# Performance work log

Measured on AMD Instinct MI355X. Metric: run time of the kernel, lower is better.

The kernel has to match this reference:

```python
import jax, jax.numpy as jnp
import numpy as np

EPS = 1e-7  # tf.keras.backend.epsilon()
ROUTINGS = 3


def squash(s):
    # s: [B, J, D]
    n2 = jnp.sum(s * s, axis=-1, keepdims=True) + EPS
    return (n2 / (1.0 + n2)) * s / jnp.sqrt(n2)


def setup_inputs() -> dict:
    key = jax.random.key(0)
    k1, k2 = jax.random.split(key)
    B, I, P = 64, 2048, 16   # batch, input_num_capsules, input_dim_capsules
    J, D = 32, 16            # num_capsules, dim_capsules (must equal P per source matmul)
    inputs = jax.random.normal(k1, (B, I, P), dtype=jnp.float32)
    W = jax.random.normal(k2, (I, J, P, D), dtype=jnp.float32) * 0.05  # glorot-ish scale
    return {"inputs": inputs, "W": W}


def reference(inputs, W):
    # tf.matmul(W_tiled, inputs_tiled): u_hat[b,i,j,d] = sum_p W[i,j,d,p] * inputs[b,i,p]
    u_hat = jnp.einsum('bip,ijdp->bijd', inputs, W)  # [B, I, J, D]
    B, I, J, _ = u_hat.shape
    b = jnp.zeros((B, I, J), dtype=u_hat.dtype)
    v = None
    for r in range(ROUTINGS):
        c = jax.nn.softmax(b, axis=2)                  # [B, I, J]
        s = jnp.einsum('bij,bijd->bjd', c, u_hat)      # [B, J, D]
        v = squash(s)
        if r < ROUTINGS - 1:
            b = b + jnp.einsum('bijd,bjd->bij', u_hat, v)
    return v
```

## Files before the change

### kernel.cpp

```cpp
#include <hip/hip_runtime.h>
#include <hip/hip_bf16.h>
#include <stdint.h>


namespace {
constexpr int B_ = 64;
constexpr int I_ = 2048;
constexpr int P_ = 16;
constexpr int J_ = 32;
constexpr int D_ = 16;
constexpr int CI_ = 128;

__device__ __forceinline__ float bflo(uint32_t v) {
  union { uint32_t u; float f; } z; z.u = v << 16; return z.f;
}
__device__ __forceinline__ float bfhi(uint32_t v) {
  union { uint32_t u; float f; } z; z.u = v & 0xffff0000u; return z.f;
}

__global__ __launch_bounds__(256) void k_uhat(const float* __restrict__ x,
                                              const float* __restrict__ W,
                                              __hip_bfloat162* __restrict__ uhat) {
  const int i = blockIdx.x;
  const int t = threadIdx.x;
  __shared__ float xs[B_][P_];
  {
    const int b = t >> 2, c = t & 3;
    const float4 v = *reinterpret_cast<const float4*>(
        x + (size_t)b * (I_ * P_) + (size_t)i * P_ + c * 4);
    *reinterpret_cast<float4*>(&xs[b][c * 4]) = v;
  }
  float w0[P_], w1[P_];
  const float* Wi = W + (size_t)i * (J_ * D_ * P_);
#pragma unroll
  for (int c = 0; c < 4; ++c) {
    *reinterpret_cast<float4*>(&w0[c * 4]) =
        *reinterpret_cast<const float4*>(Wi + (2 * t + 0) * P_ + c * 4);
    *reinterpret_cast<float4*>(&w1[c * 4]) =
        *reinterpret_cast<const float4*>(Wi + (2 * t + 1) * P_ + c * 4);
  }
  __syncthreads();
  __hip_bfloat162* dst = uhat + (size_t)i * (J_ * D_ / 2) + t;
#pragma unroll 4
  for (int b = 0; b < B_; ++b) {
    const float4* xb = reinterpret_cast<const float4*>(&xs[b][0]);
    const float4 x0 = xb[0], x1 = xb[1], x2 = xb[2], x3 = xb[3];
    const float xr[P_] = {x0.x, x0.y, x0.z, x0.w, x1.x, x1.y, x1.z, x1.w,
                          x2.x, x2.y, x2.z, x2.w, x3.x, x3.y, x3.z, x3.w};
    float a0 = 0.f, a1 = 0.f;
#pragma unroll
    for (int p = 0; p < P_; ++p) {
      a0 = fmaf(xr[p], w0[p], a0);
      a1 = fmaf(xr[p], w1[p], a1);
    }
    __hip_bfloat162 pk;
    pk.x = __float2bfloat16(a0);
    pk.y = __float2bfloat16(a1);
    dst[(size_t)b * (I_ * J_ * D_ / 2)] = pk;
  }
}

__global__ __launch_bounds__(256) void k_route(const uint4* __restrict__ uhat,
                                               const float* __restrict__ vsum,
                                               float* __restrict__ s) {
  const int b = blockIdx.y;
  const int i0 = blockIdx.x * CI_;
  const int t = threadIdx.x;
  const int lane = t & 63;
  const int wave = t >> 6;
  const int sub = lane >> 5;
  const int j = lane & 31;

  float vr[D_];
  {
    const float4* vp = reinterpret_cast<const float4*>(vsum + ((size_t)b * J_ + j) * D_);
#pragma unroll
    for (int c = 0; c < 4; ++c) {
      const float4 v = vp[c];
      vr[c * 4 + 0] = v.x; vr[c * 4 + 1] = v.y;
      vr[c * 4 + 2] = v.z; vr[c * 4 + 3] = v.w;
    }
  }
  float acc[D_];
#pragma unroll
  for (int d = 0; d < D_; ++d) acc[d] = 0.f;

  for (int it = 0; it < CI_ / 8; ++it) {
    const int i = i0 + it * 8 + wave * 2 + sub;
    const uint4* up = uhat + (((size_t)b * I_ + i) * J_ + j) * 2;
    const uint4 q0 = up[0], q1 = up[1];
    float u[D_];
    u[0] = bflo(q0.x);  u[1] = bfhi(q0.x);  u[2] = bflo(q0.y);  u[3] = bfhi(q0.y);
    u[4] = bflo(q0.z);  u[5] = bfhi(q0.z);  u[6] = bflo(q0.w);  u[7] = bfhi(q0.w);
    u[8] = bflo(q1.x);  u[9] = bfhi(q1.x);  u[10] = bflo(q1.y); u[11] = bfhi(q1.y);
    u[12] = bflo(q1.z); u[13] = bfhi(q1.z); u[14] = bflo(q1.w); u[15] = bfhi(q1.w);

    float lg = 0.f;
#pragma unroll
    for (int d = 0; d < D_; ++d) lg = fmaf(u[d], vr[d], lg);
    float m = lg;
#pragma unroll
    for (int off = 16; off > 0; off >>= 1) m = fmaxf(m, __shfl_xor(m, off, 32));
    const float e = __expf(lg - m);
    float sm = e;
#pragma unroll
    for (int off = 16; off > 0; off >>= 1) sm += __shfl_xor(sm, off, 32);
    const float c = e / sm;
#pragma unroll
    for (int d = 0; d < D_; ++d) acc[d] = fmaf(c, u[d], acc[d]);
  }
#pragma unroll
  for (int d = 0; d < D_; ++d) acc[d] += __shfl_xor(acc[d], 32, 64);

  __shared__ float sp[4][J_][D_ + 1];
  if (sub == 0) {
#pragma unroll
    for (int d = 0; d < D_; ++d) sp[wave][j][d] = acc[d];
  }
  __syncthreads();
  for (int k = t; k < J_ * D_; k += 256) {
    const int jj = k >> 4, dd = k & 15;
    atomicAdd(s + (size_t)b * (J_ * D_) + k,
              sp[0][jj][dd] + sp[1][jj][dd] + sp[2][jj][dd] + sp[3][jj][dd]);
  }
}

__global__ __launch_bounds__(256) void k_squash(const float* __restrict__ s,
                                                float* __restrict__ vsum,
                                                float* __restrict__ out) {
  const int r = blockIdx.x * 256 + threadIdx.x;
  if (r >= B_ * J_) return;
  const float4* sp = reinterpret_cast<const float4*>(s + (size_t)r * D_);
  float4 a[4] = {sp[0], sp[1], sp[2], sp[3]};
  float n2 = 1e-7f;
#pragma unroll
  for (int c = 0; c < 4; ++c)
    n2 += a[c].x * a[c].x + a[c].y * a[c].y + a[c].z * a[c].z + a[c].w * a[c].w;
  const float sc = n2 / ((1.f + n2) * sqrtf(n2));
#pragma unroll
  for (int c = 0; c < 4; ++c) {
    a[c].x *= sc; a[c].y *= sc; a[c].z *= sc; a[c].w *= sc;
  }
  if (vsum) {
    float4* vp = reinterpret_cast<float4*>(vsum + (size_t)r * D_);
#pragma unroll
    for (int c = 0; c < 4; ++c) {
      float4 v = vp[c];
      v.x += a[c].x; v.y += a[c].y; v.z += a[c].z; v.w += a[c].w;
      vp[c] = v;
    }
  }
  if (out) {
    float4* op = reinterpret_cast<float4*>(out + (size_t)r * D_);
#pragma unroll
    for (int c = 0; c < 4; ++c) op[c] = a[c];
  }
}

}

extern "C" void kernel_launch(void* const* d_in, const int* in_sizes, int n_in,
                              void* d_out, int out_size, void* d_ws, size_t ws_size,
                              hipStream_t stream) {
  const float* x = (const float*)d_in[0];
  const float* W = (const float*)d_in[1];
  float* out = (float*)d_out;

  char* ws = (char*)d_ws;
  __hip_bfloat162* uhat = (__hip_bfloat162*)ws;
  const size_t UHAT_BYTES = (size_t)B_ * I_ * J_ * D_ * 2;
  float* s0 = (float*)(ws + UHAT_BYTES);
  float* s1 = s0 + B_ * J_ * D_;
  float* s2 = s1 + B_ * J_ * D_;
  float* vsum = s2 + B_ * J_ * D_;

  hipMemsetAsync(s0, 0, (size_t)4 * B_ * J_ * D_ * sizeof(float), stream);

  k_uhat<<<I_, 256, 0, stream>>>(x, W, uhat);

  const dim3 rg(I_ / CI_, B_);
  k_route<<<rg, 256, 0, stream>>>((const uint4*)uhat, vsum, s0);
  k_squash<<<(B_ * J_ + 255) / 256, 256, 0, stream>>>(s0, vsum, nullptr);
  k_route<<<rg, 256, 0, stream>>>((const uint4*)uhat, vsum, s1);
  k_squash<<<(B_ * J_ + 255) / 256, 256, 0, stream>>>(s1, vsum, nullptr);
  k_route<<<rg, 256, 0, stream>>>((const uint4*)uhat, vsum, s2);
  k_squash<<<(B_ * J_ + 255) / 256, 256, 0, stream>>>(s2, nullptr, out);
}
```

Measured before the change: 211.0 us.

## Use bf16 MFMA for u_hat, specialize uniform first routing, drop softmax max

```diff
diff --git a/kernel.cpp b/kernel.cpp
--- a/kernel.cpp
+++ b/kernel.cpp
@@ -9,7 +9,11 @@
 constexpr int P_ = 16;
 constexpr int J_ = 32;
 constexpr int D_ = 16;
-constexpr int CI_ = 128;
+constexpr int CI_ = 64;
+constexpr int ROWS_ = J_ * D_;
+
+using short8 = __attribute__((ext_vector_type(8))) short;
+using f32x4  = __attribute__((ext_vector_type(4))) float;
 
 __device__ __forceinline__ float bflo(uint32_t v) {
   union { uint32_t u; float f; } z; z.u = v << 16; return z.f;
@@ -17,49 +21,94 @@
 __device__ __forceinline__ float bfhi(uint32_t v) {
   union { uint32_t u; float f; } z; z.u = v & 0xffff0000u; return z.f;
 }
+__device__ __forceinline__ uint16_t f2bf(float f) {
+  uint32_t u = __float_as_uint(f);
+  u += 0x7fffu + ((u >> 16) & 1u);
+  return (uint16_t)(u >> 16);
+}
 
 __global__ __launch_bounds__(256) void k_uhat(const float* __restrict__ x,
                                               const float* __restrict__ W,
-                                              __hip_bfloat162* __restrict__ uhat) {
+                                              uint16_t* __restrict__ uhat) {
   const int i = blockIdx.x;
   const int t = threadIdx.x;
-  __shared__ float xs[B_][P_];
-  {
-    const int b = t >> 2, c = t & 3;
-    const float4 v = *reinterpret_cast<const float4*>(
-        x + (size_t)b * (I_ * P_) + (size_t)i * P_ + c * 4);
-    *reinterpret_cast<float4*>(&xs[b][c * 4]) = v;
-  }
-  float w0[P_], w1[P_];
-  const float* Wi = W + (size_t)i * (J_ * D_ * P_);
-#pragma unroll
-  for (int c = 0; c < 4; ++c) {
-    *reinterpret_cast<float4*>(&w0[c * 4]) =
-        *reinterpret_cast<const float4*>(Wi + (2 * t + 0) * P_ + c * 4);
-    *reinterpret_cast<float4*>(&w1[c * 4]) =
-        *reinterpret_cast<const float4*>(Wi + (2 * t + 1) * P_ + c * 4);
-  }
-  __syncthreads();
-  __hip_bfloat162* dst = uhat + (size_t)i * (J_ * D_ / 2) + t;
-#pragma unroll 4
-  for (int b = 0; b < B_; ++b) {
-    const float4* xb = reinterpret_cast<const float4*>(&xs[b][0]);
-    const float4 x0 = xb[0], x1 = xb[1], x2 = xb[2], x3 = xb[3];
-    const float xr[P_] = {x0.x, x0.y, x0.z, x0.w, x1.x, x1.y, x1.z, x1.w,
-                          x2.x, x2.y, x2.z, x2.w, x3.x, x3.y, x3.z, x3.w};
-    float a0 = 0.f, a1 = 0.f;
-#pragma unroll
-    for (int p = 0; p < P_; ++p) {
-      a0 = fmaf(xr[p], w0[p], a0);
-      a1 = fmaf(xr[p], w1[p], a1);
-    }
-    __hip_bfloat162 pk;
-    pk.x = __float2bfloat16(a0);
-    pk.y = __float2bfloat16(a1);
-    dst[(size_t)b * (I_ * J_ * D_ / 2)] = pk;
-  }
-}
-
+  const int w = t >> 6;
+  const int l = t & 63;
+  const int g = l >> 4;
+  const int r16 = l & 15;
+
+  short8 af[4];
+#pragma unroll
+  for (int m = 0; m < 4; ++m) {
+    short8 f;
+#pragma unroll
+    for (int e = 0; e < 8; ++e) f[e] = 0;
+    if (g < 2) {
+      const float* ap = x + (size_t)(16 * m + r16) * (I_ * P_) + (size_t)i * P_ + 8 * g;
+      const float4 u0 = *reinterpret_cast<const float4*>(ap);
+      const float4 u1 = *reinterpret_cast<const float4*>(ap + 4);
+      f[0] = (short)f2bf(u0.x); f[1] = (short)f2bf(u0.y);
+      f[2] = (short)f2bf(u0.z); f[3] = (short)f2bf(u0.w);
+      f[4] = (short)f2bf(u1.x); f[5] = (short)f2bf(u1.y);
+      f[6] = (short)f2bf(u1.z); f[7] = (short)f2bf(u1.w);
+    }
+    af[m] = f;
+  }
+
+  const float* Wi = W + (size_t)i * (ROWS_ * P_);
+  uint16_t* out_i = uhat + (size_t)i * ROWS_;
+
+#pragma unroll
+  for (int rr = 0; rr < 4; ++rr) {
+    short8 bf[2];
+#pragma unroll
+    for (int tt = 0; tt < 2; ++tt) {
+      const int n = 8 * w + 2 * rr + tt;
+      short8 f;
+#pragma unroll
+      for (int e = 0; e < 8; ++e) f[e] = 0;
+      if (g < 2) {
+        const float* bp = Wi + (size_t)(16 * n + r16) * P_ + 8 * g;
+        const float4 u0 = *reinterpret_cast<const float4*>(bp);
+        const float4 u1 = *reinterpret_cast<const float4*>(bp + 4);
+        f[0] = (short)f2bf(u0.x); f[1] = (short)f2bf(u0.y);
+        f[2] = (short)f2bf(u0.z); f[3] = (short)f2bf(u0.w);
+        f[4] = (short)f2bf(u1.x); f[5] = (short)f2bf(u1.y);
+        f[6] = (short)f2bf(u1.z); f[7] = (short)f2bf(u1.w);
+      }
+      bf[tt] = f;
+    }
+
+    f32x4 acc[4][2];
+#pragma unroll
+    for (int m = 0; m < 4; ++m)
+#pragma unroll
+      for (int tt = 0; tt < 2; ++tt) {
+        acc[m][tt][0] = 0.f; acc[m][tt][1] = 0.f;
+        acc[m][tt][2] = 0.f; acc[m][tt][3] = 0.f;
+      }
+
+#pragma unroll
+    for (int m = 0; m < 4; ++m)
+#pragma unroll
+      for (int tt = 0; tt < 2; ++tt)
+        acc[m][tt] = __builtin_amdgcn_mfma_f32_16x16x32_bf16(af[m], bf[tt], acc[m][tt], 0, 0, 0);
+
+#pragma unroll
+    for (int m = 0; m < 4; ++m)
+#pragma unroll
+      for (int tt = 0; tt < 2; ++tt) {
+        const int n = 8 * w + 2 * rr + tt;
+#pragma unroll
+        for (int r = 0; r < 4; ++r) {
+          const int b = 16 * m + 4 * g + r;
+          out_i[(size_t)b * (I_ * ROWS_) + 16 * n + r16] = f2bf(acc[m][tt][r]);
+        }
+      }
+  }
+}
+
+template <bool UNIFORM>
 __global__ __launch_bounds__(256) void k_route(const uint4* __restrict__ uhat,
                                                const float* __restrict__ vsum,
                                                float* __restrict__ s) {
@@ -72,19 +121,20 @@
   const int j = lane & 31;
 
   float vr[D_];
-  {
+  if constexpr (!UNIFORM) {
     const float4* vp = reinterpret_cast<const float4*>(vsum + ((size_t)b * J_ + j) * D_);
 #pragma unroll
-    for (int c = 0; c < 4; ++c) {
-      const float4 v = vp[c];
-      vr[c * 4 + 0] = v.x; vr[c * 4 + 1] = v.y;
-      vr[c * 4 + 2] = v.z; vr[c * 4 + 3] = v.w;
+    for (int c4 = 0; c4 < 4; ++c4) {
+      const float4 v = vp[c4];
+      vr[c4 * 4 + 0] = v.x; vr[c4 * 4 + 1] = v.y;
+      vr[c4 * 4 + 2] = v.z; vr[c4 * 4 + 3] = v.w;
     }
   }
   float acc[D_];
 #pragma unroll
   for (int d = 0; d < D_; ++d) acc[d] = 0.f;
 
+#pragma unroll 2
   for (int it = 0; it < CI_ / 8; ++it) {
     const int i = i0 + it * 8 + wave * 2 + sub;
     const uint4* up = uhat + (((size_t)b * I_ + i) * J_ + j) * 2;
@@ -95,19 +145,25 @@
     u[8] = bflo(q1.x);  u[9] = bfhi(q1.x);  u[10] = bflo(q1.y); u[11] = bfhi(q1.y);
     u[12] = bflo(q1.z); u[13] = bfhi(q1.z); u[14] = bflo(q1.w); u[15] = bfhi(q1.w);
 
-    float lg = 0.f;
-#pragma unroll
-    for (int d = 0; d < D_; ++d) lg = fmaf(u[d], vr[d], lg);
-    float m = lg;
-#pragma unroll
-    for (int off = 16; off > 0; off >>= 1) m = fmaxf(m, __shfl_xor(m, off, 32));
-    const float e = __expf(lg - m);
-    float sm = e;
-#pragma unroll
-    for (int off = 16; off > 0; off >>= 1) sm += __shfl_xor(sm, off, 32);
-    const float c = e / sm;
-#pragma unroll
-    for (int d = 0; d < D_; ++d) acc[d] = fmaf(c, u[d], acc[d]);
+    if constexpr (UNIFORM) {
+#pragma unroll
+      for (int d = 0; d < D_; ++d) acc[d] += u[d];
+    } else {
+      float lg = 0.f;
+#pragma unroll
+      for (int d = 0; d < D_; ++d) lg = fmaf(u[d], vr[d], lg);
+      const float e = __expf(lg);
+      float sm = e;
+#pragma unroll
+      for (int off = 16; off > 0; off >>= 1) sm += __shfl_xor(sm, off, 32);
+      const float c = e * __builtin_amdgcn_rcpf(sm);
+#pragma unroll
+      for (int d = 0; d < D_; ++d) acc[d] = fmaf(c, u[d], acc[d]);
+    }
+  }
+  if constexpr (UNIFORM) {
+#pragma unroll
+    for (int d = 0; d < D_; ++d) acc[d] *= (1.0f / J_);
   }
 #pragma unroll
   for (int d = 0; d < D_; ++d) acc[d] += __shfl_xor(acc[d], 32, 64);
@@ -167,8 +223,8 @@
   float* out = (float*)d_out;
 
   char* ws = (char*)d_ws;
-  __hip_bfloat162* uhat = (__hip_bfloat162*)ws;
-  const size_t UHAT_BYTES = (size_t)B_ * I_ * J_ * D_ * 2;
+  uint16_t* uhat = (uint16_t*)ws;
+  const size_t UHAT_BYTES = (size_t)B_ * I_ * ROWS_ * 2;
   float* s0 = (float*)(ws + UHAT_BYTES);
   float* s1 = s0 + B_ * J_ * D_;
   float* s2 = s1 + B_ * J_ * D_;
@@ -179,10 +235,10 @@
   k_uhat<<<I_, 256, 0, stream>>>(x, W, uhat);
 
   const dim3 rg(I_ / CI_, B_);
-  k_route<<<rg, 256, 0, stream>>>((const uint4*)uhat, vsum, s0);
+  k_route<true><<<rg, 256, 0, stream>>>((const uint4*)uhat, vsum, s0);
   k_squash<<<(B_ * J_ + 255) / 256, 256, 0, stream>>>(s0, vsum, nullptr);
-  k_route<<<rg, 256, 0, stream>>>((const uint4*)uhat, vsum, s1);
+  k_route<false><<<rg, 256, 0, stream>>>((const uint4*)uhat, vsum, s1);
   k_squash<<<(B_ * J_ + 255) / 256, 256, 0, stream>>>(s1, vsum, nullptr);
-  k_route<<<rg, 256, 0, stream>>>((const uint4*)uhat, vsum, s2);
+  k_route<false><<<rg, 256, 0, stream>>>((const uint4*)uhat, vsum, s2);
   k_squash<<<(B_ * J_ + 255) / 256, 256, 0, stream>>>(s2, nullptr, out);
 }
```

Measured after the change: 259.8 us. 23.1% more time.

## Use MFMA fp16 for u_hat, fuse squash into routing, specialize passes

Applied to the files above, without the earlier changes.

```diff
diff --git a/kernel.cpp b/kernel.cpp
--- a/kernel.cpp
+++ b/kernel.cpp
@@ -9,60 +9,107 @@
 constexpr int P_ = 16;
 constexpr int J_ = 32;
 constexpr int D_ = 16;
-constexpr int CI_ = 128;
-
-__device__ __forceinline__ float bflo(uint32_t v) {
-  union { uint32_t u; float f; } z; z.u = v << 16; return z.f;
-}
-__device__ __forceinline__ float bfhi(uint32_t v) {
-  union { uint32_t u; float f; } z; z.u = v & 0xffff0000u; return z.f;
+constexpr int CI_ = 64;
+constexpr int ROWS_ = J_ * D_;
+
+using half8 = __attribute__((ext_vector_type(8))) _Float16;
+using h2    = __attribute__((ext_vector_type(2))) _Float16;
+using f32x4 = __attribute__((ext_vector_type(4))) float;
+
+__device__ __forceinline__ uint32_t pkh2(float a, float b) {
+  union { h2 h; uint32_t u; } z;
+  z.h[0] = (_Float16)a; z.h[1] = (_Float16)b;
+  return z.u;
+}
+__device__ __forceinline__ h2 as_h2(uint32_t u) {
+  union { uint32_t uu; h2 h; } z; z.uu = u; return z.h;
+}
+__device__ __forceinline__ float dot2acc(h2 a, h2 b, float c) {
+#if __has_builtin(__builtin_amdgcn_fdot2)
+  return __builtin_amdgcn_fdot2(a, b, c, false);
+#else
+  return fmaf((float)a[0], (float)b[0], fmaf((float)a[1], (float)b[1], c));
+#endif
 }
 
 __global__ __launch_bounds__(256) void k_uhat(const float* __restrict__ x,
                                               const float* __restrict__ W,
-                                              __hip_bfloat162* __restrict__ uhat) {
+                                              uint16_t* __restrict__ uhat) {
   const int i = blockIdx.x;
   const int t = threadIdx.x;
-  __shared__ float xs[B_][P_];
-  {
-    const int b = t >> 2, c = t & 3;
-    const float4 v = *reinterpret_cast<const float4*>(
-        x + (size_t)b * (I_ * P_) + (size_t)i * P_ + c * 4);
-    *reinterpret_cast<float4*>(&xs[b][c * 4]) = v;
-  }
-  float w0[P_], w1[P_];
-  const float* Wi = W + (size_t)i * (J_ * D_ * P_);
-#pragma unroll
-  for (int c = 0; c < 4; ++c) {
-    *reinterpret_cast<float4*>(&w0[c * 4]) =
-        *reinterpret_cast<const float4*>(Wi + (2 * t + 0) * P_ + c * 4);
-    *reinterpret_cast<float4*>(&w1[c * 4]) =
-        *reinterpret_cast<const float4*>(Wi + (2 * t + 1) * P_ + c * 4);
-  }
-  __syncthreads();
-  __hip_bfloat162* dst = uhat + (size_t)i * (J_ * D_ / 2) + t;
-#pragma unroll 4
-  for (int b = 0; b < B_; ++b) {
-    const float4* xb = reinterpret_cast<const float4*>(&xs[b][0]);
-    const float4 x0 = xb[0], x1 = xb[1], x2 = xb[2], x3 = xb[3];
-    const float xr[P_] = {x0.x, x0.y, x0.z, x0.w, x1.x, x1.y, x1.z, x1.w,
-                          x2.x, x2.y, x2.z, x2.w, x3.x, x3.y, x3.z, x3.w};
-    float a0 = 0.f, a1 = 0.f;
-#pragma unroll
-    for (int p = 0; p < P_; ++p) {
-      a0 = fmaf(xr[p], w0[p], a0);
-      a1 = fmaf(xr[p], w1[p], a1);
-    }
-    __hip_bfloat162 pk;
-    pk.x = __float2bfloat16(a0);
-    pk.y = __float2bfloat16(a1);
-    dst[(size_t)b * (I_ * J_ * D_ / 2)] = pk;
-  }
-}
-
+  const int w = t >> 6;
+  const int l = t & 63;
+  const int g = l >> 4;
+  const int r16 = l & 15;
+
+  half8 bfr[4];
+#pragma unroll
+  for (int bm = 0; bm < 4; ++bm) {
+    half8 f;
+#pragma unroll
+    for (int e = 0; e < 8; ++e) f[e] = (_Float16)0.f;
+    if (g < 2) {
+      const float* bp = x + (size_t)(16 * bm + r16) * (I_ * P_) + (size_t)i * P_ + 8 * g;
+      const float4 u0 = *reinterpret_cast<const float4*>(bp);
+      const float4 u1 = *reinterpret_cast<const float4*>(bp + 4);
+      f[0] = (_Float16)u0.x; f[1] = (_Float16)u0.y; f[2] = (_Float16)u0.z; f[3] = (_Float16)u0.w;
+      f[4] = (_Float16)u1.x; f[5] = (_Float16)u1.y; f[6] = (_Float16)u1.z; f[7] = (_Float16)u1.w;
+    }
+    bfr[bm] = f;
+  }
+
+  const float* Wi = W + (size_t)i * (ROWS_ * P_);
+  uint16_t* out_i = uhat + (size_t)i * ROWS_;
+
+#pragma unroll
+  for (int nn = 0; nn < 8; ++nn) {
+    const int n = 8 * w + nn;
+    half8 af;
+#pragma unroll
+    for (int e = 0; e < 8; ++e) af[e] = (_Float16)0.f;
+    if (g < 2) {
+      const float* ap = Wi + (size_t)(16 * n + r16) * P_ + 8 * g;
+      const float4 u0 = *reinterpret_cast<const float4*>(ap);
+      const float4 u1 = *reinterpret_cast<const float4*>(ap + 4);
+      af[0] = (_Float16)u0.x; af[1] = (_Float16)u0.y; af[2] = (_Float16)u0.z; af[3] = (_Float16)u0.w;
+      af[4] = (_Float16)u1.x; af[5] = (_Float16)u1.y; af[6] = (_Float16)u1.z; af[7] = (_Float16)u1.w;
+    }
+
+#pragma unroll
+    for (int bm = 0; bm < 4; ++bm) {
+      f32x4 acc;
+      acc[0] = 0.f; acc[1] = 0.f; acc[2] = 0.f; acc[3] = 0.f;
+      acc = __builtin_amdgcn_mfma_f32_16x16x32_f16(af, bfr[bm], acc, 0, 0, 0);
+      const int b = 16 * bm + r16;
+      const int ro = 16 * n + 4 * g;
+      uint2 st;
+      st.x = pkh2(acc[0], acc[1]);
+      st.y = pkh2(acc[2], acc[3]);
+      *reinterpret_cast<uint2*>(out_i + (size_t)b * (I_ * ROWS_) + ro) = st;
+    }
+  }
+}
+
+__device__ __forceinline__ void load_squash_add(const float* __restrict__ p, float* v) {
+  const float4* sp = reinterpret_cast<const float4*>(p);
+  const float4 a0 = sp[0], a1 = sp[1], a2 = sp[2], a3 = sp[3];
+  float n2 = 1e-7f;
+  n2 += a0.x * a0.x + a0.y * a0.y + a0.z * a0.z + a0.w * a0.w;
+  n2 += a1.x * a1.x + a1.y * a1.y + a1.z * a1.z + a1.w * a1.w;
+  n2 += a2.x * a2.x + a2.y * a2.y + a2.z * a2.z + a2.w * a2.w;
+  n2 += a3.x * a3.x + a3.y * a3.y + a3.z * a3.z + a3.w * a3.w;
+  const float sc = n2 / ((1.f + n2) * sqrtf(n2));
+  v[0] += sc * a0.x;  v[1] += sc * a0.y;  v[2] += sc * a0.z;  v[3] += sc * a0.w;
+  v[4] += sc * a1.x;  v[5] += sc * a1.y;  v[6] += sc * a1.z;  v[7] += sc * a1.w;
+  v[8] += sc * a2.x;  v[9] += sc * a2.y;  v[10] += sc * a2.z; v[11] += sc * a2.w;
+  v[12] += sc * a3.x; v[13] += sc * a3.y; v[14] += sc * a3.z; v[15] += sc * a3.w;
+}
+
+template <int PASS>
 __global__ __launch_bounds__(256) void k_route(const uint4* __restrict__ uhat,
-                                               const float* __restrict__ vsum,
-                                               float* __restrict__ s) {
+                                               const float* __restrict__ s0,
+                                               const float* __restrict__ s1,
+                                               float* __restrict__ sout) {
   const int b = blockIdx.y;
   const int i0 = blockIdx.x * CI_;
   const int t = threadIdx.x;
@@ -71,43 +118,61 @@
   const int sub = lane >> 5;
   const int j = lane & 31;
 
-  float vr[D_];
-  {
-    const float4* vp = reinterpret_cast<const float4*>(vsum + ((size_t)b * J_ + j) * D_);
-#pragma unroll
-    for (int c = 0; c < 4; ++c) {
-      const float4 v = vp[c];
-      vr[c * 4 + 0] = v.x; vr[c * 4 + 1] = v.y;
-      vr[c * 4 + 2] = v.z; vr[c * 4 + 3] = v.w;
-    }
-  }
+  h2 vh[8];
+  if constexpr (PASS > 0) {
+    float v[16];
+#pragma unroll
+    for (int d = 0; d < D_; ++d) v[d] = 0.f;
+    load_squash_add(s0 + ((size_t)b * J_ + j) * D_, v);
+    if constexpr (PASS == 2) load_squash_add(s1 + ((size_t)b * J_ + j) * D_, v);
+#pragma unroll
+    for (int q = 0; q < 8; ++q) {
+      h2 hv;
+      hv[0] = (_Float16)v[2 * q];
+      hv[1] = (_Float16)v[2 * q + 1];
+      vh[q] = hv;
+    }
+  }
+
   float acc[D_];
 #pragma unroll
   for (int d = 0; d < D_; ++d) acc[d] = 0.f;
 
-  for (int it = 0; it < CI_ / 8; ++it) {
-    const int i = i0 + it * 8 + wave * 2 + sub;
-    const uint4* up = uhat + (((size_t)b * I_ + i) * J_ + j) * 2;
+  const uint4* up = uhat + (((size_t)b * I_ + i0 + wave * 2 + sub) * J_ + j) * 2;
+  const size_t step = (size_t)8 * J_ * 2;
+
+#pragma unroll 2
+  for (int it = 0; it < CI_ / 8; ++it, up += step) {
     const uint4 q0 = up[0], q1 = up[1];
-    float u[D_];
-    u[0] = bflo(q0.x);  u[1] = bfhi(q0.x);  u[2] = bflo(q0.y);  u[3] = bfhi(q0.y);
-    u[4] = bflo(q0.z);  u[5] = bfhi(q0.z);  u[6] = bflo(q0.w);  u[7] = bfhi(q0.w);
-    u[8] = bflo(q1.x);  u[9] = bfhi(q1.x);  u[10] = bflo(q1.y); u[11] = bfhi(q1.y);
-    u[12] = bflo(q1.z); u[13] = bfhi(q1.z); u[14] = bflo(q1.w); u[15] = bfhi(q1.w);
-
-    float lg = 0.f;
-#pragma unroll
-    for (int d = 0; d < D_; ++d) lg = fmaf(u[d], vr[d], lg);
-    float m = lg;
-#pragma unroll
-    for (int off = 16; off > 0; off >>= 1) m = fmaxf(m, __shfl_xor(m, off, 32));
-    const float e = __expf(lg - m);
-    float sm = e;
-#pragma unroll
-    for (int off = 16; off > 0; off >>= 1) sm += __shfl_xor(sm, off, 32);
-    const float c = e / sm;
-#pragma unroll
-    for (int d = 0; d < D_; ++d) acc[d] = fmaf(c, u[d], acc[d]);
+    const h2 u0 = as_h2(q0.x), u1 = as_h2(q0.y), u2 = as_h2(q0.z), u3 = as_h2(q0.w);
+    const h2 u4 = as_h2(q1.x), u5 = as_h2(q1.y), u6 = as_h2(q1.z), u7 = as_h2(q1.w);
+    float c;
+    if constexpr (PASS == 0) {
+      c = 1.0f;
+    } else {
+      float lg = 0.f;
+      lg = dot2acc(u0, vh[0], lg); lg = dot2acc(u1, vh[1], lg);
+      lg = dot2acc(u2, vh[2], lg); lg = dot2acc(u3, vh[3], lg);
+      lg = dot2acc(u4, vh[4], lg); lg = dot2acc(u5, vh[5], lg);
+      lg = dot2acc(u6, vh[6], lg); lg = dot2acc(u7, vh[7], lg);
+      const float e = __expf(lg);
+      float sm = e;
+#pragma unroll
+      for (int off = 16; off > 0; off >>= 1) sm += __shfl_xor(sm, off, 32);
+      c = e * __builtin_amdgcn_rcpf(sm);
+    }
+    acc[0]  = fmaf((float)u0[0], c, acc[0]);  acc[1]  = fmaf((float)u0[1], c, acc[1]);
+    acc[2]  = fmaf((float)u1[0], c, acc[2]);  acc[3]  = fmaf((float)u1[1], c, acc[3]);
+    acc[4]  = fmaf((float)u2[0], c, acc[4]);  acc[5]  = fmaf((float)u2[1], c, acc[5]);
+    acc[6]  = fmaf((float)u3[0], c, acc[6]);  acc[7]  = fmaf((float)u3[1], c, acc[7]);
+    acc[8]  = fmaf((float)u4[0], c, acc[8]);  acc[9]  = fmaf((float)u4[1], c, acc[9]);
+    acc[10] = fmaf((float)u5[0], c, acc[10]); acc[11] = fmaf((float)u5[1], c, acc[11]);
+    acc[12] = fmaf((float)u6[0], c, acc[12]); acc[13] = fmaf((float)u6[1], c, acc[13]);
+    acc[14] = fmaf((float)u7[0], c, acc[14]); acc[15] = fmaf((float)u7[1], c, acc[15]);
+  }
+  if constexpr (PASS == 0) {
+#pragma unroll
+    for (int d = 0; d < D_; ++d) acc[d] *= (1.0f / J_);
   }
 #pragma unroll
   for (int d = 0; d < D_; ++d) acc[d] += __shfl_xor(acc[d], 32, 64);
@@ -120,13 +185,12 @@
   __syncthreads();
   for (int k = t; k < J_ * D_; k += 256) {
     const int jj = k >> 4, dd = k & 15;
-    atomicAdd(s + (size_t)b * (J_ * D_) + k,
+    atomicAdd(sout + (size_t)b * (J_ * D_) + k,
               sp[0][jj][dd] + sp[1][jj][dd] + sp[2][jj][dd] + sp[3][jj][dd]);
   }
 }
 
 __global__ __launch_bounds__(256) void k_squash(const float* __restrict__ s,
-                                                float* __restrict__ vsum,
                                                 float* __restrict__ out) {
   const int r = blockIdx.x * 256 + threadIdx.x;
   if (r >= B_ * J_) return;
@@ -137,23 +201,12 @@
   for (int c = 0; c < 4; ++c)
     n2 += a[c].x * a[c].x + a[c].y * a[c].y + a[c].z * a[c].z + a[c].w * a[c].w;
   const float sc = n2 / ((1.f + n2) * sqrtf(n2));
+  float4* op = reinterpret_cast<float4*>(out + (size_t)r * D_);
 #pragma unroll
   for (int c = 0; c < 4; ++c) {
-    a[c].x *= sc; a[c].y *= sc; a[c].z *= sc; a[c].w *= sc;
-  }
-  if (vsum) {
-    float4* vp = reinterpret_cast<float4*>(vsum + (size_t)r * D_);
-#pragma unroll
-    for (int c = 0; c < 4; ++c) {
-      float4 v = vp[c];
-      v.x += a[c].x; v.y += a[c].y; v.z += a[c].z; v.w += a[c].w;
-      vp[c] = v;
-    }
-  }
-  if (out) {
-    float4* op = reinterpret_cast<float4*>(out + (size_t)r * D_);
-#pragma unroll
-    for (int c = 0; c < 4; ++c) op[c] = a[c];
+    float4 v = a[c];
+    v.x *= sc; v.y *= sc; v.z *= sc; v.w *= sc;
+    op[c] = v;
   }
 }
 
@@ -167,22 +220,19 @@
   float* out = (float*)d_out;
 
   char* ws = (char*)d_ws;
-  __hip_bfloat162* uhat = (__hip_bfloat162*)ws;
-  const size_t UHAT_BYTES = (size_t)B_ * I_ * J_ * D_ * 2;
+  uint16_t* uhat = (uint16_t*)ws;
+  const size_t UHAT_BYTES = (size_t)B_ * I_ * ROWS_ * 2;
   float* s0 = (float*)(ws + UHAT_BYTES);
   float* s1 = s0 + B_ * J_ * D_;
   float* s2 = s1 + B_ * J_ * D_;
-  float* vsum = s2 + B_ * J_ * D_;
-
-  hipMemsetAsync(s0, 0, (size_t)4 * B_ * J_ * D_ * sizeof(float), stream);
+
+  hipMemsetAsync(s0, 0, (size_t)3 * B_ * J_ * D_ * sizeof(float), stream);
 
   k_uhat<<<I_, 256, 0, stream>>>(x, W, uhat);
 
   const dim3 rg(I_ / CI_, B_);
-  k_route<<<rg, 256, 0, stream>>>((const uint4*)uhat, vsum, s0);
-  k_squash<<<(B_ * J_ + 255) / 256, 256, 0, stream>>>(s0, vsum, nullptr);
-  k_route<<<rg, 256, 0, stream>>>((const uint4*)uhat, vsum, s1);
-  k_squash<<<(B_ * J_ + 255) / 256, 256, 0, stream>>>(s1, vsum, nullptr);
-  k_route<<<rg, 256, 0, stream>>>((const uint4*)uhat, vsum, s2);
-  k_squash<<<(B_ * J_ + 255) / 256, 256, 0, stream>>>(s2, nullptr, out);
-}
+  k_route<0><<<rg, 256, 0, stream>>>((const uint4*)uhat, nullptr, nullptr, s0);
+  k_route<1><<<rg, 256, 0, stream>>>((const uint4*)uhat, s0, nullptr, s1);
+  k_route<2><<<rg, 256, 0, stream>>>((const uint4*)uhat, s0, s1, s2);
+  k_squash<<<(B_ * J_ + 255) / 256, 256, 0, stream>>>(s2, out);
+}
```

Measured after the change: 302.4 us. +43.3%, slower.
